# Optimization experiments

Measured on AMD Instinct MI355X. Metric: run time of the kernel, lower is better.

The kernel has to match this reference:

```python
import jax, jax.numpy as jnp
import numpy as np

B, L, HID, H = 2, 2048, 1024, 16
HD = HID // H
MAX_REL = 2


def setup_inputs() -> dict:
    key = jax.random.key(0)
    ks = jax.random.split(key, 16)
    s = 0.02
    return {
        "query": jax.random.normal(ks[0], (B, L, HID), jnp.float32),
        "key": jax.random.normal(ks[1], (B, L, HID), jnp.float32),
        "value": jax.random.normal(ks[2], (B, L, HID), jnp.float32),
        "Wq": jax.random.normal(ks[3], (HID, HID), jnp.float32) * s,
        "bq": jnp.zeros((HID,), jnp.float32),
        "Wk": jax.random.normal(ks[4], (HID, HID), jnp.float32) * s,
        "bk": jnp.zeros((HID,), jnp.float32),
        "Wv": jax.random.normal(ks[5], (HID, HID), jnp.float32) * s,
        "bv": jnp.zeros((HID,), jnp.float32),
        "Wo": jax.random.normal(ks[6], (HID, HID), jnp.float32) * s,
        "bo": jnp.zeros((HID,), jnp.float32),
        "rel_k_table": jax.random.normal(ks[7], (2 * MAX_REL + 1, HD), jnp.float32) * s,
        "rel_v_table": jax.random.normal(ks[8], (2 * MAX_REL + 1, HD), jnp.float32) * s,
    }


def _rel_embeddings(table, len_q, len_k):
    # Shaw-style clipped relative position lookup -> [len_q, len_k, head_dim]
    dist = jnp.arange(len_k)[None, :] - jnp.arange(len_q)[:, None]
    idx = jnp.clip(dist, -MAX_REL, MAX_REL) + MAX_REL
    return table[idx]


def reference(query, key, value, Wq, bq, Wk, bk, Wv, bv, Wo, bo, rel_k_table, rel_v_table):
    b, lq, hid = query.shape
    lk = key.shape[1]
    q = (query @ Wq.T + bq).reshape(b, lq, H, HD)   # [b, lq, h, hd]
    k = (key @ Wk.T + bk).reshape(b, lk, H, HD)     # [b, lk, h, hd]
    v = (value @ Wv.T + bv).reshape(b, lk, H, HD)   # [b, lk, h, hd]

    rk = _rel_embeddings(rel_k_table, lq, lk)       # [lq, lk, hd]
    rv = _rel_embeddings(rel_v_table, lq, lk)       # [lq, lk, hd]

    attn1 = jnp.einsum('bqhd,bkhd->bhqk', q, k)
    attn2 = jnp.einsum('bqhd,qkd->bhqk', q, rk)
    # NOTE: original code averages the two scores and does NOT divide by sqrt(head_dim)
    attn = jax.nn.softmax((attn1 + attn2) * 0.5, axis=-1)

    w1 = jnp.einsum('bhqk,bkhd->bhqd', attn, v)
    w2 = jnp.einsum('bhqk,qkd->bhqd', attn, rv)
    x = (w1 + w2).transpose(0, 2, 1, 3).reshape(b, lq, hid)
    return x @ Wo.T + bo
```

## Files before the change

### kernel.cpp

```cpp
#include <hip/hip_runtime.h>
#include <hip/hip_bf16.h>
#include <math.h>

typedef __attribute__((ext_vector_type(8))) short bf16x8;
typedef __attribute__((ext_vector_type(4))) float f32x4;
typedef __attribute__((ext_vector_type(16))) float f32x16;

constexpr int Bc   = 2;
constexpr int Lc   = 2048;
constexpr int HIDc = 1024;
constexpr int Hc   = 16;
constexpr int HDc  = 64;
constexpr int Mc   = 4096;

__device__ __forceinline__ ushort f2bf(float f) {
  uint u = __float_as_uint(f);
  u += 0x7fff + ((u >> 16) & 1);
  return (ushort)(u >> 16);
}

__device__ __forceinline__ void gload16(const ushort* g, ushort* l) {
  __builtin_amdgcn_global_load_lds(
      (const __attribute__((address_space(1))) uint*)(const void*)g,
      (__attribute__((address_space(3))) uint*)(void*)l, 16, 0, 0);
}

__device__ __forceinline__ uint cvtpk(float lo, float hi_) {
  uint r;
  asm("v_cvt_pk_bf16_f32 %0, %1, %2" : "=v"(r) : "v"(lo), "v"(hi_));
  return r;
}
__device__ __forceinline__ void pswap(uint &a, uint &b) {
  asm("v_permlane32_swap_b32 %0, %1" : "+v"(a), "+v"(b));
}

__global__ __launch_bounds__(256)
void cvt7(const float* __restrict__ q, const float* __restrict__ k,
          const float* __restrict__ v, const float* __restrict__ wq,
          const float* __restrict__ wk, const float* __restrict__ wv,
          const float* __restrict__ wo,
          ushort* dq_, ushort* dk, ushort* dv,
          ushort* dwq, ushort* dwk, ushort* dwv, ushort* dwo)
{
  int blk = blockIdx.x;
  const float* s; ushort* d; int off;
  if      (blk < 2048) { s = q;  d = dq_; off = blk; }
  else if (blk < 4096) { s = k;  d = dk;  off = blk - 2048; }
  else if (blk < 6144) { s = v;  d = dv;  off = blk - 4096; }
  else if (blk < 6656) { s = wq; d = dwq; off = blk - 6144; }
  else if (blk < 7168) { s = wk; d = dwk; off = blk - 6656; }
  else if (blk < 7680) { s = wv; d = dwv; off = blk - 7168; }
  else                 { s = wo; d = dwo; off = blk - 7680; }
  size_t i = (size_t)off * 2048 + threadIdx.x * 8;
  float4 a = *(const float4*)(s + i);
  float4 b = *(const float4*)(s + i + 4);
  ushort t[8] = { f2bf(a.x), f2bf(a.y), f2bf(a.z), f2bf(a.w),
                  f2bf(b.x), f2bf(b.y), f2bf(b.z), f2bf(b.w) };
  *(uint4*)(d + i) = *(uint4*)t;
}

__global__ __launch_bounds__(512)
void gemm_bf16(const ushort* __restrict__ A, const ushort* __restrict__ Bw,
               const float* __restrict__ bias, float* __restrict__ Cf,
               ushort* __restrict__ Cb, int M, int N, int K, int mode)
{
  __shared__ ushort As[2][128*32];
  __shared__ ushort Bs[2][128*32];
  const int tid  = threadIdx.x;
  const int lane = tid & 63;
  const int w    = tid >> 6;
  const int g    = lane >> 4;
  const int lc   = lane & 15;
  const int wr   = w >> 2;
  const int wc   = w & 3;
  const int row0 = blockIdx.y * 128;
  const int col0 = blockIdx.x * 128;

  const int sr  = tid >> 2;
  const int sc_ = tid & 3;
  const int scg = sc_ ^ ((sr >> 1) & 3);
  const ushort* pA = A  + (size_t)(row0 + sr) * K + scg * 8;
  const ushort* pB = Bw + (size_t)(col0 + sr) * K + scg * 8;

  int aoff[4], boff[2];
  #pragma unroll
  for (int mi = 0; mi < 4; ++mi) {
    int r = wr*64 + mi*16 + lc;
    aoff[mi] = r*32 + (g ^ ((r >> 1) & 3)) * 8;
  }
  #pragma unroll
  for (int ni = 0; ni < 2; ++ni) {
    int r = wc*32 + ni*16 + lc;
    boff[ni] = r*32 + (g ^ ((r >> 1) & 3)) * 8;
  }

  f32x4 acc[4][2];
  #pragma unroll
  for (int mi = 0; mi < 4; ++mi)
    #pragma unroll
    for (int ni = 0; ni < 2; ++ni) acc[mi][ni] = (f32x4){0.f,0.f,0.f,0.f};

  gload16(pA, &As[0][tid*8]);
  gload16(pB, &Bs[0][tid*8]);
  __syncthreads();

  const int NT = K >> 5;
  for (int t = 0; t < NT; ++t) {
    if (t + 1 < NT) {
      int k0 = (t + 1) << 5;
      gload16(pA + k0, &As[(t+1)&1][tid*8]);
      gload16(pB + k0, &Bs[(t+1)&1][tid*8]);
    }
    const ushort* as = As[t & 1];
    const ushort* bs = Bs[t & 1];
    bf16x8 af[4], bfr[2];
    #pragma unroll
    for (int mi = 0; mi < 4; ++mi) af[mi] = *(const bf16x8*)&as[aoff[mi]];
    #pragma unroll
    for (int ni = 0; ni < 2; ++ni) bfr[ni] = *(const bf16x8*)&bs[boff[ni]];
    #pragma unroll
    for (int mi = 0; mi < 4; ++mi)
      #pragma unroll
      for (int ni = 0; ni < 2; ++ni)
        acc[mi][ni] = __builtin_amdgcn_mfma_f32_16x16x32_bf16(af[mi], bfr[ni], acc[mi][ni], 0, 0, 0);
    __syncthreads();
  }

  const int colbase = col0 + wc*32;
  if (mode == 0) {
    #pragma unroll
    for (int mi = 0; mi < 4; ++mi) {
      int row = row0 + wr*64 + mi*16 + 4*g;
      #pragma unroll
      for (int ni = 0; ni < 2; ++ni) {
        int col = colbase + ni*16 + lc;
        float bb = bias[col];
        #pragma unroll
        for (int reg = 0; reg < 4; ++reg)
          Cf[(size_t)(row + reg) * N + col] = acc[mi][ni][reg] + bb;
      }
    }
  } else if (mode == 1) {
    #pragma unroll
    for (int mi = 0; mi < 4; ++mi) {
      int row = row0 + wr*64 + mi*16 + 4*g;
      int b = row >> 11, qq = row & 2047;
      #pragma unroll
      for (int ni = 0; ni < 2; ++ni) {
        int col = colbase + ni*16 + lc;
        int h = col >> 6, d = col & 63;
        float bb = bias[col];
        size_t base = (((size_t)b*Hc + h)*Lc + qq)*HDc + d;
        #pragma unroll
        for (int reg = 0; reg < 4; ++reg)
          Cb[base + (size_t)reg*HDc] = f2bf(acc[mi][ni][reg] + bb);
      }
    }
  } else {
    #pragma unroll
    for (int mi = 0; mi < 4; ++mi) {
      int row = row0 + wr*64 + mi*16 + 4*g;
      int b = row >> 11, kk = row & 2047;
      #pragma unroll
      for (int ni = 0; ni < 2; ++ni) {
        int col = colbase + ni*16 + lc;
        int h = col >> 6, d = col & 63;
        float bb = bias[col];
        ushort t4[4];
        #pragma unroll
        for (int reg = 0; reg < 4; ++reg) t4[reg] = f2bf(acc[mi][ni][reg] + bb);
        *(uint2*)&Cb[(((size_t)b*Hc + h)*HDc + d)*Lc + kk] = *(uint2*)t4;
      }
    }
  }
}

__global__ __launch_bounds__(256)
void attn_mfma32(const ushort* __restrict__ Qc, const ushort* __restrict__ Kc,
                 const ushort* __restrict__ Vt, const float* __restrict__ relk,
                 const float* __restrict__ relv, ushort* __restrict__ X)
{
  __shared__ ushort KVs[2][9216];
  __shared__ float epi[4][6][32];

  const int tid  = threadIdx.x;
  const int w    = tid >> 6;
  const int lane = tid & 63;
  const int lq   = lane & 31;
  const int hi   = lane >> 5;

  const int blk  = blockIdx.x;
  const int qblk = blk & 15;
  const int bh   = blk >> 4;
  const int b    = bh >> 4;
  const int h    = bh & 15;
  const int qw   = qblk*128 + w*32;
  const int qabs = qw + lq;

  const ushort* Kbh = Kc + (size_t)bh*Lc*HDc;
  const ushort* Vbh = Vt + (size_t)bh*HDc*Lc;

  bf16x8 qf[4];
  const ushort* qbase = Qc + ((size_t)bh*Lc + qabs)*HDc + 8*hi;
  #pragma unroll
  for (int s = 0; s < 4; ++s) qf[s] = *(const bf16x8*)(qbase + 16*s);

  f32x16 dc;
  #pragma unroll
  for (int i = 0; i < 16; ++i) dc[i] = 0.f;
  #pragma unroll
  for (int s = 0; s < 4; ++s) {
    union { ushort u[8]; bf16x8 v; } rf;
    #pragma unroll
    for (int j = 0; j < 8; ++j) rf.u[j] = 0;
    if (lq < 5) {
      #pragma unroll
      for (int j = 0; j < 8; ++j) rf.u[j] = f2bf(relk[lq*HDc + 16*s + 8*hi + j]);
    }
    dc = __builtin_amdgcn_mfma_f32_32x32x16_bf16(rf.v, qf[s], dc, 0, 0, 0);
  }
  float o0 = __shfl_xor(dc[0], 32), o1 = __shfl_xor(dc[1], 32),
        o2 = __shfl_xor(dc[2], 32), o3 = __shfl_xor(dc[3], 32);
  float dqh0, dqh1, dqh2, dqh3, dqh4;
  if (hi == 0) { dqh0 = dc[0]; dqh1 = dc[1]; dqh2 = dc[2]; dqh3 = dc[3]; dqh4 = o0; }
  else         { dqh0 = o0;    dqh1 = o1;    dqh2 = o2;    dqh3 = o3;    dqh4 = dc[0]; }
  dqh0 *= 0.5f; dqh1 *= 0.5f; dqh2 *= 0.5f; dqh3 *= 0.5f; dqh4 *= 0.5f;

  f32x16 acc0, acc1;
  #pragma unroll
  for (int i = 0; i < 16; ++i) { acc0[i] = 0.f; acc1[i] = 0.f; }
  float lsum = 0.f, llo = 0.f, e1 = 0.f, e2 = 0.f, e3 = 0.f;

  auto stage = [&](ushort* dst, int k0) {
    #pragma unroll
    for (int cc = 0; cc < 5; ++cc) {
      int idx = cc*4 + w;
      if (idx < 9) {
        int p = idx*64 + lane;
        int row = p/9, ch = p - row*9;
        gload16(Kbh + (size_t)(k0 + row)*HDc + ch*8, dst + idx*512 + lane*8);
      } else if (idx < 18) {
        int p = (idx - 9)*64 + lane;
        int row = p/9, ch = p - row*9;
        gload16(Vbh + (size_t)row*Lc + k0 + ch*8, dst + idx*512 + lane*8);
      }
    }
  };

  auto group = [&](const f32x16& c, int kb, const ushort* vb_, int g) {
    float p[16];
    if (kb >= qw + 33) {
      #pragma unroll
      for (int r = 0; r < 16; ++r) { p[r] = __expf(0.5f*c[r] + dqh4); lsum += p[r]; }
    } else if (kb + 33 <= qw) {
      #pragma unroll
      for (int r = 0; r < 16; ++r) { p[r] = __expf(0.5f*c[r] + dqh0); lsum += p[r]; llo += p[r]; }
    } else {
      int bnum = kb + 4*hi - qabs;
      #pragma unroll
      for (int r = 0; r < 16; ++r) {
        int dist = bnum + ((r & 3) + 8*(r >> 2));
        float dq = dist <= -2 ? dqh0 : (dist >= 2 ? dqh4 :
                   (dist == -1 ? dqh1 : (dist == 0 ? dqh2 : dqh3)));
        float pp = __expf(0.5f*c[r] + dq);
        p[r] = pp; lsum += pp;
        llo += (dist <= -2) ? pp : 0.f;
        e1  += (dist == -1) ? pp : 0.f;
        e2  += (dist == 0)  ? pp : 0.f;
        e3  += (dist == 1)  ? pp : 0.f;
      }
    }
    #pragma unroll
    for (int s2 = 0; s2 < 2; ++s2) {
      uint X0 = cvtpk(p[8*s2+0], p[8*s2+1]);
      uint X1 = cvtpk(p[8*s2+2], p[8*s2+3]);
      uint Y0 = cvtpk(p[8*s2+4], p[8*s2+5]);
      uint Y1 = cvtpk(p[8*s2+6], p[8*s2+7]);
      pswap(X0, Y0); pswap(X1, Y1);
      union { uint u[4]; bf16x8 v; } aw;
      aw.u[0] = X0; aw.u[1] = X1; aw.u[2] = Y0; aw.u[3] = Y1;
      bf16x8 vf0 = *(const bf16x8*)&vb_[(lq)     *72 + (4*g + 2*s2 + hi)*8];
      bf16x8 vf1 = *(const bf16x8*)&vb_[(32 + lq)*72 + (4*g + 2*s2 + hi)*8];
      acc0 = __builtin_amdgcn_mfma_f32_32x32x16_bf16(aw.v, vf0, acc0, 0, 0, 0);
      acc1 = __builtin_amdgcn_mfma_f32_32x32x16_bf16(aw.v, vf1, acc1, 0, 0, 0);
    }
  };

  stage(KVs[0], 0);
  __syncthreads();

  for (int t = 0; t < Lc/64; ++t) {
    const ushort* kb_ = KVs[t & 1];
    const ushort* vb_ = kb_ + 4608;
    if (t + 1 < Lc/64) stage(KVs[(t+1) & 1], (t+1)*64);
    const int k0 = t*64;

    bf16x8 kfa[4], kfb[4];
    #pragma unroll
    for (int s = 0; s < 4; ++s) {
      kfa[s] = *(const bf16x8*)&kb_[(lq)     *72 + (hi + 2*s)*8];
      kfb[s] = *(const bf16x8*)&kb_[(32 + lq)*72 + (hi + 2*s)*8];
    }
    f32x16 c0, c1;
    #pragma unroll
    for (int i = 0; i < 16; ++i) { c0[i] = 0.f; c1[i] = 0.f; }
    #pragma unroll
    for (int s = 0; s < 4; ++s)
      c0 = __builtin_amdgcn_mfma_f32_32x32x16_bf16(kfa[s], qf[s], c0, 0, 0, 0);
    #pragma unroll
    for (int s = 0; s < 4; ++s)
      c1 = __builtin_amdgcn_mfma_f32_32x32x16_bf16(kfb[s], qf[s], c1, 0, 0, 0);

    group(c0, k0,      vb_, 0);
    group(c1, k0 + 32, vb_, 1);
    __syncthreads();
  }

  float Ls = lsum + __shfl_xor(lsum, 32);
  float Lo = llo  + __shfl_xor(llo, 32);
  float E1 = e1   + __shfl_xor(e1, 32);
  float E2 = e2   + __shfl_xor(e2, 32);
  float E3 = e3   + __shfl_xor(e3, 32);
  float inv = 1.f / Ls;
  float s0 = Lo*inv, s1_ = E1*inv, s2_ = E2*inv, s3_ = E3*inv;
  float s4_ = 1.f - s0 - s1_ - s2_ - s3_;
  if (lane < 32) {
    epi[w][0][lq] = inv; epi[w][1][lq] = s0;  epi[w][2][lq] = s1_;
    epi[w][3][lq] = s2_; epi[w][4][lq] = s3_; epi[w][5][lq] = s4_;
  }
  float rvv[5][2];
  #pragma unroll
  for (int r = 0; r < 5; ++r) {
    rvv[r][0] = relv[r*HDc + lq];
    rvv[r][1] = relv[r*HDc + 32 + lq];
  }
  asm volatile("s_waitcnt lgkmcnt(0)" ::: "memory");
  #pragma unroll
  for (int r = 0; r < 16; ++r) {
    int qloc = ((r & 3) + 8*(r >> 2)) + 4*hi;
    float iv = epi[w][0][qloc], t0 = epi[w][1][qloc], t1 = epi[w][2][qloc],
          t2 = epi[w][3][qloc], t3 = epi[w][4][qloc], t4 = epi[w][5][qloc];
    size_t rowb = ((size_t)b*Lc + qw + qloc)*HIDc + h*HDc;
    float v0 = acc0[r]*iv + t0*rvv[0][0] + t1*rvv[1][0] + t2*rvv[2][0]
             + t3*rvv[3][0] + t4*rvv[4][0];
    float v1 = acc1[r]*iv + t0*rvv[0][1] + t1*rvv[1][1] + t2*rvv[2][1]
             + t3*rvv[3][1] + t4*rvv[4][1];
    X[rowb + lq]      = f2bf(v0);
    X[rowb + 32 + lq] = f2bf(v1);
  }
}

extern "C" void kernel_launch(void* const* d_in, const int* in_sizes, int n_in,
                              void* d_out, int out_size, void* d_ws, size_t ws_size,
                              hipStream_t stream) {
  const float* query = (const float*)d_in[0];
  const float* key   = (const float*)d_in[1];
  const float* value = (const float*)d_in[2];
  const float* Wq    = (const float*)d_in[3];
  const float* bq    = (const float*)d_in[4];
  const float* Wk    = (const float*)d_in[5];
  const float* bk    = (const float*)d_in[6];
  const float* Wv    = (const float*)d_in[7];
  const float* bv    = (const float*)d_in[8];
  const float* Wo    = (const float*)d_in[9];
  const float* bo    = (const float*)d_in[10];
  const float* relk  = (const float*)d_in[11];
  const float* relv  = (const float*)d_in[12];
  float* out = (float*)d_out;

  size_t S2 = (size_t)Mc * HIDc;
  ushort* base = (ushort*)d_ws;
  ushort* R0 = base;
  ushort* R1 = base + S2;
  ushort* R2 = base + 2*S2;
  ushort* R3 = base + 3*S2;
  ushort* R4 = base + 4*S2;
  ushort* W5 = base + 5*S2;
  ushort* WqB = W5, *WkB = W5 + S2/4, *WvB = W5 + 2*(S2/4), *WoB = W5 + 3*(S2/4);

  cvt7<<<8192, 256, 0, stream>>>(query, key, value, Wq, Wk, Wv, Wo,
                                 R0, R1, R2, WqB, WkB, WvB, WoB);

  dim3 grid_g(HIDc / 128, Mc / 128);
  gemm_bf16<<<grid_g, 512, 0, stream>>>(R1, WkB, bk, nullptr, R3, Mc, HIDc, HIDc, 1);
  gemm_bf16<<<grid_g, 512, 0, stream>>>(R0, WqB, bq, nullptr, R1, Mc, HIDc, HIDc, 1);
  gemm_bf16<<<grid_g, 512, 0, stream>>>(R2, WvB, bv, nullptr, R4, Mc, HIDc, HIDc, 2);

  attn_mfma32<<<Bc * Hc * (Lc / 128), 256, 0, stream>>>(R1, R3, R4, relk, relv, R0);

  gemm_bf16<<<grid_g, 512, 0, stream>>>(R0, WoB, bo, out, nullptr, Mc, HIDc, HIDc, 0);
}
```

Measured before the change: 176.8 us.

## Shrink attention blocks to two waves, swizzle block order, use exp2 and setprio

The attention kernel now launches 128-thread blocks covering 64 queries instead of 256 threads covering 128, which doubles the grid to 1024 blocks. Block indices are swizzled so that consecutive blocks go to different heads. The softmax folds 0.5*log2(e) into a single FMA feeding a native exp2, and the uniform-region row sums use a tree reduction. MFMA sections are wrapped in s_setprio to favour matrix issue. Smaller blocks improve occupancy and load balance, but each block reloads the same K/V tiles, so K/V traffic per query doubles.

```diff
diff --git a/kernel.cpp b/kernel.cpp
--- a/kernel.cpp
+++ b/kernel.cpp
@@ -175,13 +175,13 @@
   }
 }
 
-__global__ __launch_bounds__(256)
+__global__ __launch_bounds__(128)
 void attn_mfma32(const ushort* __restrict__ Qc, const ushort* __restrict__ Kc,
                  const ushort* __restrict__ Vt, const float* __restrict__ relk,
                  const float* __restrict__ relv, ushort* __restrict__ X)
 {
   __shared__ ushort KVs[2][9216];
-  __shared__ float epi[4][6][32];
+  __shared__ float epi[2][6][32];
 
   const int tid  = threadIdx.x;
   const int w    = tid >> 6;
@@ -189,13 +189,15 @@
   const int lq   = lane & 31;
   const int hi   = lane >> 5;
 
-  const int blk  = blockIdx.x;
-  const int qblk = blk & 15;
-  const int bh   = blk >> 4;
+  const int swz  = (blockIdx.x & 7) * 128 + (blockIdx.x >> 3);
+  const int qblk = swz & 31;
+  const int bh   = swz >> 5;
   const int b    = bh >> 4;
   const int h    = bh & 15;
-  const int qw   = qblk*128 + w*32;
+  const int qw   = qblk*64 + w*32;
   const int qabs = qw + lq;
+
+  constexpr float C2 = 0.72134752f;
 
   const ushort* Kbh = Kc + (size_t)bh*Lc*HDc;
   const ushort* Vbh = Vt + (size_t)bh*HDc*Lc;
@@ -224,7 +226,7 @@
   float dqh0, dqh1, dqh2, dqh3, dqh4;
   if (hi == 0) { dqh0 = dc[0]; dqh1 = dc[1]; dqh2 = dc[2]; dqh3 = dc[3]; dqh4 = o0; }
   else         { dqh0 = o0;    dqh1 = o1;    dqh2 = o2;    dqh3 = o3;    dqh4 = dc[0]; }
-  dqh0 *= 0.5f; dqh1 *= 0.5f; dqh2 *= 0.5f; dqh3 *= 0.5f; dqh4 *= 0.5f;
+  dqh0 *= C2; dqh1 *= C2; dqh2 *= C2; dqh3 *= C2; dqh4 *= C2;
 
   f32x16 acc0, acc1;
   #pragma unroll
@@ -233,28 +235,32 @@
 
   auto stage = [&](ushort* dst, int k0) {
     #pragma unroll
-    for (int cc = 0; cc < 5; ++cc) {
-      int idx = cc*4 + w;
-      if (idx < 9) {
-        int p = idx*64 + lane;
-        int row = p/9, ch = p - row*9;
-        gload16(Kbh + (size_t)(k0 + row)*HDc + ch*8, dst + idx*512 + lane*8);
-      } else if (idx < 18) {
-        int p = (idx - 9)*64 + lane;
-        int row = p/9, ch = p - row*9;
-        gload16(Vbh + (size_t)row*Lc + k0 + ch*8, dst + idx*512 + lane*8);
+    for (int i = 0; i < 9; ++i) {
+      int c = i*128 + tid;
+      if (c < 576) {
+        int row = c/9, ch = c - row*9;
+        gload16(Kbh + (size_t)(k0 + row)*HDc + ch*8, dst + c*8);
+      } else {
+        int cv = c - 576;
+        int row = cv/9, ch = cv - row*9;
+        gload16(Vbh + (size_t)row*Lc + k0 + ch*8, dst + c*8);
       }
     }
   };
 
   auto group = [&](const f32x16& c, int kb, const ushort* vb_, int g) {
     float p[16];
-    if (kb >= qw + 33) {
-      #pragma unroll
-      for (int r = 0; r < 16; ++r) { p[r] = __expf(0.5f*c[r] + dqh4); lsum += p[r]; }
-    } else if (kb + 33 <= qw) {
-      #pragma unroll
-      for (int r = 0; r < 16; ++r) { p[r] = __expf(0.5f*c[r] + dqh0); lsum += p[r]; llo += p[r]; }
+    const bool allhi = (kb >= qw + 33);
+    const bool alllo = (kb + 33 <= qw);
+    if (allhi | alllo) {
+      const float dq = allhi ? dqh4 : dqh0;
+      #pragma unroll
+      for (int r = 0; r < 16; ++r)
+        p[r] = __builtin_amdgcn_exp2f(__builtin_fmaf(c[r], C2, dq));
+      float gs = (((p[0]+p[1]) + (p[2]+p[3])) + ((p[4]+p[5]) + (p[6]+p[7])))
+               + (((p[8]+p[9]) + (p[10]+p[11])) + ((p[12]+p[13]) + (p[14]+p[15])));
+      lsum += gs;
+      if (alllo) llo += gs;
     } else {
       int bnum = kb + 4*hi - qabs;
       #pragma unroll
@@ -262,7 +268,7 @@
         int dist = bnum + ((r & 3) + 8*(r >> 2));
         float dq = dist <= -2 ? dqh0 : (dist >= 2 ? dqh4 :
                    (dist == -1 ? dqh1 : (dist == 0 ? dqh2 : dqh3)));
-        float pp = __expf(0.5f*c[r] + dq);
+        float pp = __builtin_amdgcn_exp2f(__builtin_fmaf(c[r], C2, dq));
         p[r] = pp; lsum += pp;
         llo += (dist <= -2) ? pp : 0.f;
         e1  += (dist == -1) ? pp : 0.f;
@@ -281,8 +287,10 @@
       aw.u[0] = X0; aw.u[1] = X1; aw.u[2] = Y0; aw.u[3] = Y1;
       bf16x8 vf0 = *(const bf16x8*)&vb_[(lq)     *72 + (4*g + 2*s2 + hi)*8];
       bf16x8 vf1 = *(const bf16x8*)&vb_[(32 + lq)*72 + (4*g + 2*s2 + hi)*8];
+      __builtin_amdgcn_s_setprio(1);
       acc0 = __builtin_amdgcn_mfma_f32_32x32x16_bf16(aw.v, vf0, acc0, 0, 0, 0);
       acc1 = __builtin_amdgcn_mfma_f32_32x32x16_bf16(aw.v, vf1, acc1, 0, 0, 0);
+      __builtin_amdgcn_s_setprio(0);
     }
   };
 
@@ -304,12 +312,14 @@
     f32x16 c0, c1;
     #pragma unroll
     for (int i = 0; i < 16; ++i) { c0[i] = 0.f; c1[i] = 0.f; }
+    __builtin_amdgcn_s_setprio(1);
     #pragma unroll
     for (int s = 0; s < 4; ++s)
       c0 = __builtin_amdgcn_mfma_f32_32x32x16_bf16(kfa[s], qf[s], c0, 0, 0, 0);
     #pragma unroll
     for (int s = 0; s < 4; ++s)
       c1 = __builtin_amdgcn_mfma_f32_32x32x16_bf16(kfb[s], qf[s], c1, 0, 0, 0);
+    __builtin_amdgcn_s_setprio(0);
 
     group(c0, k0,      vb_, 0);
     group(c1, k0 + 32, vb_, 1);
@@ -386,7 +396,7 @@
   gemm_bf16<<<grid_g, 512, 0, stream>>>(R0, WqB, bq, nullptr, R1, Mc, HIDc, HIDc, 1);
   gemm_bf16<<<grid_g, 512, 0, stream>>>(R2, WvB, bv, nullptr, R4, Mc, HIDc, HIDc, 2);
 
-  attn_mfma32<<<Bc * Hc * (Lc / 128), 256, 0, stream>>>(R1, R3, R4, relk, relv, R0);
+  attn_mfma32<<<Bc * Hc * (Lc / 64), 128, 0, stream>>>(R1, R3, R4, relk, relv, R0);
 
   gemm_bf16<<<grid_g, 512, 0, stream>>>(R0, WoB, bo, out, nullptr, Mc, HIDc, HIDc, 0);
 }
```

Result: no change. 175.9 us (-0.5%).
